# Kernel tuning notes

Measured on AMD Instinct MI355X. Metric: run time of the kernel, lower is better.

Reference implementation:

```python
import jax, jax.numpy as jnp
import numpy as np

DIM = 1024
NUM_HEADS = 16
HEAD_DIM = DIM // NUM_HEADS


def _rope(x):
    # x: (B*H, L, hd). ESM-style rotary embedding with rotate_half.
    L, hd = x.shape[1], x.shape[2]
    inv_freq = 1.0 / (10000.0 ** (jnp.arange(0, hd, 2, dtype=jnp.float32) / hd))
    t = jnp.arange(L, dtype=jnp.float32)
    freqs = t[:, None] * inv_freq[None, :]          # (L, hd/2)
    emb = jnp.concatenate([freqs, freqs], axis=-1)   # (L, hd)
    cos, sin = jnp.cos(emb), jnp.sin(emb)
    x1, x2 = jnp.split(x, 2, axis=-1)
    rot = jnp.concatenate([-x2, x1], axis=-1)
    return x * cos + rot * sin


def setup_inputs() -> dict:
    key = jax.random.key(0)
    ks = jax.random.split(key, 10)
    L, N, D = 2048, 1, DIM
    query = jax.random.normal(ks[0], (L, N, D), dtype=jnp.float32)
    asym_ids = jnp.sort(jax.random.randint(ks[1], (N, L), 0, 4), axis=-1)
    s = 0.02
    wq = s * jax.random.normal(ks[2], (D, D), dtype=jnp.float32)
    wk = s * jax.random.normal(ks[3], (D, D), dtype=jnp.float32)
    wv = s * jax.random.normal(ks[4], (D, D), dtype=jnp.float32)
    wo = s * jax.random.normal(ks[5], (D, D), dtype=jnp.float32)
    bq = s * jax.random.normal(ks[6], (D,), dtype=jnp.float32)
    bk = s * jax.random.normal(ks[7], (D,), dtype=jnp.float32)
    bv = s * jax.random.normal(ks[8], (D,), dtype=jnp.float32)
    bo = s * jax.random.normal(ks[9], (D,), dtype=jnp.float32)
    return {"query": query, "asym_ids": asym_ids, "wq": wq, "bq": bq,
            "wk": wk, "bk": bk, "wv": wv, "bv": bv, "wo": wo, "bo": bo}


def reference(query, asym_ids, wq, bq, wk, bk, wv, bv, wo, bo):
    L, N, D = query.shape
    H, hd = NUM_HEADS, HEAD_DIM
    scaling = 1.0 / np.sqrt(hd)

    q = (query @ wq.T + bq) * scaling
    k = query @ wk.T + bk
    v = query @ wv.T + bv

    def to_bh(x):  # (L, N, D) -> (N*H, L, hd)
        return x.reshape(L, N * H, hd).transpose(1, 0, 2)

    q, k, v = to_bh(q), to_bh(k), to_bh(v)

    # raw scores (pre-RoPE), rpe scores (post-RoPE)
    raw = jnp.einsum('ble,bme->blm', q, k).reshape(N, H, L, L)
    qr, kr = _rope(q), _rope(k)
    rpe = jnp.einsum('ble,bme->blm', qr, kr).reshape(N, H, L, L)

    avg = jnp.mean(rpe - raw, axis=(0, 1), keepdims=True)          # (1,1,L,L)
    asym_mask = asym_ids[:, :, None] == asym_ids[:, None, :]        # (N,L,L)
    attn_weights = jnp.where(asym_mask[:, None], rpe, raw + avg)    # (N,H,L,L)

    probs = jax.nn.softmax(attn_weights, axis=-1)
    attn = jnp.einsum('nhlm,nhme->nhle', probs, v.reshape(N, H, L, hd))
    attn = attn.transpose(2, 0, 1, 3).reshape(L, N, D)
    out = attn @ wo.T + bo
    attn_weights_avg = jnp.mean(probs, axis=1)  # (N, L, L)
    return out, attn_weights_avg
```

## Files before the change

### kernel.cpp

```cpp
#include <hip/hip_runtime.h>
#include <hip/hip_bf16.h>

#define L 2048
#define D 1024
#define NH 16
#define HD 64
#define SPLIT 4
#define JCH (L / SPLIT)
#define LOG2E 1.4426950408889634f

typedef __attribute__((ext_vector_type(8))) short bf16x8;
typedef __attribute__((ext_vector_type(4))) float f32x4;

#define MFMA(a, b, c) __builtin_amdgcn_mfma_f32_16x16x32_bf16(a, b, c, 0, 0, 0)

__device__ __forceinline__ short f2bf(float x) {
  __hip_bfloat16 h = __float2bfloat16(x);
  return *reinterpret_cast<short*>(&h);
}

__device__ __forceinline__ void gll16(const void* g, void* l) {
  __builtin_amdgcn_global_load_lds(
      (const __attribute__((address_space(1))) void*)(uintptr_t)g,
      (__attribute__((address_space(3))) void*)(unsigned)(uintptr_t)l, 16, 0, 0);
}

__global__ void prep_kernel(const float* __restrict__ q,
                            const float* __restrict__ w0, const float* __restrict__ w1,
                            const float* __restrict__ w2, const float* __restrict__ w3,
                            float* __restrict__ costab, float* __restrict__ sintab,
                            short* __restrict__ dq, short* __restrict__ d0,
                            short* __restrict__ d1, short* __restrict__ d2,
                            short* __restrict__ d3) {
  int i = blockIdx.x * 256 + threadIdx.x;
  if (i < 65536) {
    int t = i >> 5, fi = i & 31;
    float f = exp2f(-(float)fi * (13.287712379549449f / 32.0f));
    float ang = (float)t * f;
    costab[i] = cosf(ang);
    sintab[i] = sinf(ang);
    return;
  }
  int i2 = i - 65536;
  const float* src;
  short* dst;
  int off;
  if (i2 < L * D / 4) {
    src = q; dst = dq; off = i2;
  } else {
    int j = i2 - L * D / 4;
    int seg = j >> 18;
    off = j & (262144 - 1);
    src = seg == 0 ? w0 : seg == 1 ? w1 : seg == 2 ? w2 : w3;
    dst = seg == 0 ? d0 : seg == 1 ? d1 : seg == 2 ? d2 : d3;
  }
  float4 v = ((const float4*)src)[off];
  short4 o;
  o.x = f2bf(v.x); o.y = f2bf(v.y); o.z = f2bf(v.z); o.w = f2bf(v.w);
  ((short4*)dst)[off] = o;
}

__global__ __launch_bounds__(256) void proj3_kernel(
    const short* __restrict__ X,
    const short* __restrict__ Wq, const short* __restrict__ Wk, const short* __restrict__ Wv,
    const float* __restrict__ bq, const float* __restrict__ bk, const float* __restrict__ bv,
    const float* __restrict__ costab, const float* __restrict__ sintab,
    short* __restrict__ Qs, short* __restrict__ QRb, short* __restrict__ Kbb,
    short* __restrict__ KRb, short* __restrict__ Vt) {
  int mode = blockIdx.z;
  const short* W = mode == 0 ? Wq : (mode == 1 ? Wk : Wv);
  const float* bias = mode == 0 ? bq : (mode == 1 ? bk : bv);
  short* out_main = mode == 0 ? Qs : (mode == 1 ? Kbb : Vt);
  short* out_rope = mode == 0 ? QRb : KRb;

  int w = threadIdx.x >> 6, lane = threadIdx.x & 63;
  int c = lane & 15, g = lane >> 4;
  int wi0 = blockIdx.y * 128 + (w >> 1) * 64;
  int wj0 = blockIdx.x * 128 + (w & 1) * 64;

  f32x4 acc[4][4];
#pragma unroll
  for (int m = 0; m < 4; ++m)
#pragma unroll
    for (int n = 0; n < 4; ++n) acc[m][n] = (f32x4){0.f, 0.f, 0.f, 0.f};

  for (int k0 = 0; k0 < D; k0 += 32) {
    bf16x8 aF[4], bF[4];
#pragma unroll
    for (int m = 0; m < 4; ++m)
      aF[m] = *(const bf16x8*)(X + (size_t)(wi0 + m * 16 + c) * D + k0 + g * 8);
#pragma unroll
    for (int n = 0; n < 4; ++n)
      bF[n] = *(const bf16x8*)(W + (size_t)(wj0 + n * 16 + c) * D + k0 + g * 8);
#pragma unroll
    for (int m = 0; m < 4; ++m)
#pragma unroll
      for (int n = 0; n < 4; ++n) acc[m][n] = MFMA(aF[m], bF[n], acc[m][n]);
  }

  float scale = (mode == 0) ? 0.125f * LOG2E : 1.0f;
#pragma unroll
  for (int m = 0; m < 4; ++m) {
#pragma unroll
    for (int r = 0; r < 4; ++r) {
      int i = wi0 + m * 16 + g * 4 + r;
      float v4[4];
#pragma unroll
      for (int n = 0; n < 4; ++n)
        v4[n] = (acc[m][n][r] + bias[wj0 + n * 16 + c]) * scale;
      if (mode == 2) {
#pragma unroll
        for (int n = 0; n < 4; ++n) {
          int col = wj0 + n * 16 + c;
          out_main[(size_t)col * L + i] = f2bf(v4[n]);
        }
      } else {
#pragma unroll
        for (int n = 0; n < 4; ++n) {
          int col = wj0 + n * 16 + c;
          out_main[(size_t)i * D + col] = f2bf(v4[n]);
          float rot = (n < 2) ? -v4[n + 2] : v4[n - 2];
          int fidx = i * 32 + (n & 1) * 16 + c;
          float vr = v4[n] * costab[fidx] + rot * sintab[fidx];
          out_rope[(size_t)i * D + col] = f2bf(vr);
        }
      }
    }
  }
}

__global__ __launch_bounds__(256) void avg_kernel(
    const short* __restrict__ QR, const short* __restrict__ KR,
    const short* __restrict__ Qs, const short* __restrict__ Kb,
    const int* __restrict__ ids, f32x4* __restrict__ avg4) {
  int ib = blockIdx.y * 128, jb = blockIdx.x * 64;
  if (ids[ib] == ids[ib + 127] && ids[jb] == ids[jb + 63] && ids[ib] == ids[jb])
    return;

  int w = threadIdx.x >> 6, lane = threadIdx.x & 63;
  int c = lane & 15, g = lane >> 4;
  int wi0 = ib + (w >> 1) * 64;
  int wj0 = jb + (w & 1) * 32;

  f32x4 acc1[4][2], acc2[4][2];
#pragma unroll
  for (int m = 0; m < 4; ++m)
#pragma unroll
    for (int n = 0; n < 2; ++n) {
      acc1[m][n] = (f32x4){0.f, 0.f, 0.f, 0.f};
      acc2[m][n] = (f32x4){0.f, 0.f, 0.f, 0.f};
    }

  for (int k0 = 0; k0 < D; k0 += 32) {
    bf16x8 aF[4], a2F[4], bF[2], b2F[2];
#pragma unroll
    for (int m = 0; m < 4; ++m) {
      aF[m] = *(const bf16x8*)(QR + (size_t)(wi0 + m * 16 + c) * D + k0 + g * 8);
      a2F[m] = *(const bf16x8*)(Qs + (size_t)(wi0 + m * 16 + c) * D + k0 + g * 8);
    }
#pragma unroll
    for (int n = 0; n < 2; ++n) {
      bF[n] = *(const bf16x8*)(KR + (size_t)(wj0 + n * 16 + c) * D + k0 + g * 8);
      b2F[n] = *(const bf16x8*)(Kb + (size_t)(wj0 + n * 16 + c) * D + k0 + g * 8);
    }
#pragma unroll
    for (int m = 0; m < 4; ++m)
#pragma unroll
      for (int n = 0; n < 2; ++n) {
        acc1[m][n] = MFMA(aF[m], bF[n], acc1[m][n]);
        acc2[m][n] = MFMA(a2F[m], b2F[n], acc2[m][n]);
      }
  }

#pragma unroll
  for (int m = 0; m < 4; ++m)
#pragma unroll
    for (int n = 0; n < 2; ++n) {
      int j = wj0 + n * 16 + c;
      f32x4 o;
#pragma unroll
      for (int r = 0; r < 4; ++r) o[r] = (acc1[m][n][r] - acc2[m][n][r]) * 0.0625f;
      avg4[(size_t)(((wi0 + m * 16) >> 2) + g) * L + j] = o;
    }
}

__global__ __launch_bounds__(256) void flash3_kernel(
    const short* __restrict__ Qs, const short* __restrict__ Kb,
    const short* __restrict__ QR, const short* __restrict__ KR,
    const short* __restrict__ Vt, const f32x4* __restrict__ avg4,
    const int* __restrict__ ids, float* __restrict__ m_part,
    float* __restrict__ l_part, float* __restrict__ acc_part) {
  int h = blockIdx.y, sp = blockIdx.z;
  int w = threadIdx.x >> 6, lane = threadIdx.x & 63;
  int c = lane & 15, g = lane >> 4;
  int i0 = blockIdx.x * 64 + w * 16;
  int hk = h * 64;

  __shared__ short kb_lds[2][64 * 64];
  __shared__ short kr_lds[2][64 * 64];
  __shared__ short plds[4][16][64];

  int srow = lane >> 3;
  int sxor = (lane & 7) ^ srow;
  int r0a = w * 16, r0b = w * 16 + 8;

  bf16x8 qA[2], qrA[2];
  {
    const short* qp = Qs + (size_t)(i0 + c) * D + hk + g * 8;
    const short* qrp = QR + (size_t)(i0 + c) * D + hk + g * 8;
    qA[0] = *(const bf16x8*)qp;   qA[1] = *(const bf16x8*)(qp + 32);
    qrA[0] = *(const bf16x8*)qrp; qrA[1] = *(const bf16x8*)(qrp + 32);
  }

  int idi[4];
  float mrun[4], lsum[4];
  f32x4 acc[4];
#pragma unroll
  for (int r = 0; r < 4; ++r) {
    idi[r] = ids[i0 + g * 4 + r];
    mrun[r] = -3.0e38f;
    lsum[r] = 0.f;
  }
#pragma unroll
  for (int n = 0; n < 4; ++n) acc[n] = (f32x4){0.f, 0.f, 0.f, 0.f};

  int ifirst = __shfl(idi[0], 0);
  bool iu = __all((idi[0] == idi[1]) & (idi[1] == idi[2]) & (idi[2] == idi[3]) &
                  (idi[0] == ifirst));

  const f32x4* avrow = avg4 + (size_t)((i0 >> 2) + g) * L;
  int jbase = sp * JCH;
  const int NT = JCH / 64;

  gll16(Kb + (size_t)(jbase + r0a + srow) * D + hk + sxor * 8, &kb_lds[0][r0a * 64]);
  gll16(Kb + (size_t)(jbase + r0b + srow) * D + hk + sxor * 8, &kb_lds[0][r0b * 64]);
  gll16(KR + (size_t)(jbase + r0a + srow) * D + hk + sxor * 8, &kr_lds[0][r0a * 64]);
  gll16(KR + (size_t)(jbase + r0b + srow) * D + hk + sxor * 8, &kr_lds[0][r0b * 64]);

  f32x4 avn[4];
  int idjn[4];
#pragma unroll
  for (int sub = 0; sub < 4; ++sub) {
    avn[sub] = avrow[jbase + sub * 16 + c];
    idjn[sub] = ids[jbase + sub * 16 + c];
  }
  __syncthreads();

  int cur = 0;
  for (int jt = 0; jt < NT; ++jt) {
    int jb = jbase + jt * 64;

    if (jt + 1 < NT) {
      int jn = jb + 64;
      short* kd = &kb_lds[cur ^ 1][0];
      short* rd = &kr_lds[cur ^ 1][0];
      gll16(Kb + (size_t)(jn + r0a + srow) * D + hk + sxor * 8, kd + r0a * 64);
      gll16(Kb + (size_t)(jn + r0b + srow) * D + hk + sxor * 8, kd + r0b * 64);
      gll16(KR + (size_t)(jn + r0a + srow) * D + hk + sxor * 8, rd + r0a * 64);
      gll16(KR + (size_t)(jn + r0b + srow) * D + hk + sxor * 8, rd + r0b * 64);
    }

    bf16x8 vf0[4], vf1[4];
#pragma unroll
    for (int n = 0; n < 4; ++n) {
      const short* vp = Vt + (size_t)(hk + n * 16 + c) * L + jb + g * 8;
      vf0[n] = *(const bf16x8*)vp;
      vf1[n] = *(const bf16x8*)(vp + 32);
    }

    f32x4 av[4];
    int idj[4];
#pragma unroll
    for (int sub = 0; sub < 4; ++sub) { av[sub] = avn[sub]; idj[sub] = idjn[sub]; }
    if (jt + 1 < NT) {
#pragma unroll
      for (int sub = 0; sub < 4; ++sub) {
        avn[sub] = avrow[jb + 64 + sub * 16 + c];
        idjn[sub] = ids[jb + 64 + sub * 16 + c];
      }
    }

    int jfirst = __shfl(idj[0], 0);
    bool ju = __all((idj[0] == idj[1]) & (idj[1] == idj[2]) & (idj[2] == idj[3]) &
                    (idj[0] == jfirst));

    const short* kbb = &kb_lds[cur][c * 64];
    const short* krb = &kr_lds[cur][c * 64];
    int co0 = (g ^ (c & 7)) * 8;
    int co1 = ((4 + g) ^ (c & 7)) * 8;

    float t[4][4];
    if (iu && ju && ifirst == jfirst) {
#pragma unroll
      for (int sub = 0; sub < 4; ++sub) {
        bf16x8 kr0 = *(const bf16x8*)(krb + sub * 1024 + co0);
        bf16x8 kr1 = *(const bf16x8*)(krb + sub * 1024 + co1);
        f32x4 z = (f32x4){0.f, 0.f, 0.f, 0.f};
        f32x4 rp = MFMA(qrA[1], kr1, MFMA(qrA[0], kr0, z));
#pragma unroll
        for (int r = 0; r < 4; ++r) t[sub][r] = rp[r];
      }
    } else if (iu && ju) {
#pragma unroll
      for (int sub = 0; sub < 4; ++sub) {
        bf16x8 k0 = *(const bf16x8*)(kbb + sub * 1024 + co0);
        bf16x8 k1 = *(const bf16x8*)(kbb + sub * 1024 + co1);
        f32x4 z = (f32x4){0.f, 0.f, 0.f, 0.f};
        f32x4 rw = MFMA(qA[1], k1, MFMA(qA[0], k0, z));
#pragma unroll
        for (int r = 0; r < 4; ++r) t[sub][r] = rw[r] + av[sub][r];
      }
    } else {
#pragma unroll
      for (int sub = 0; sub < 4; ++sub) {
        bf16x8 k0 = *(const bf16x8*)(kbb + sub * 1024 + co0);
        bf16x8 k1 = *(const bf16x8*)(kbb + sub * 1024 + co1);
        bf16x8 kr0 = *(const bf16x8*)(krb + sub * 1024 + co0);
        bf16x8 kr1 = *(const bf16x8*)(krb + sub * 1024 + co1);
        f32x4 z = (f32x4){0.f, 0.f, 0.f, 0.f};
        f32x4 rw = MFMA(qA[1], k1, MFMA(qA[0], k0, z));
        f32x4 rp = MFMA(qrA[1], kr1, MFMA(qrA[0], kr0, z));
#pragma unroll
        for (int r = 0; r < 4; ++r)
          t[sub][r] = (idi[r] == idj[sub]) ? rp[r] : (rw[r] + av[sub][r]);
      }
    }

    float tm[4];
#pragma unroll
    for (int r = 0; r < 4; ++r)
      tm[r] = fmaxf(fmaxf(t[0][r], t[1][r]), fmaxf(t[2][r], t[3][r]));
    bool ok = (tm[0] <= mrun[0] + 8.f) && (tm[1] <= mrun[1] + 8.f) &&
              (tm[2] <= mrun[2] + 8.f) && (tm[3] <= mrun[3] + 8.f);
    if (!__all(ok)) {
#pragma unroll
      for (int r = 0; r < 4; ++r) {
        float m2 = tm[r];
#pragma unroll
        for (int d = 1; d < 16; d <<= 1) m2 = fmaxf(m2, __shfl_xor(m2, d));
        float mn = fmaxf(mrun[r], m2);
        float so = exp2f(mrun[r] - mn);
        mrun[r] = mn;
        lsum[r] *= so;
#pragma unroll
        for (int n = 0; n < 4; ++n) acc[n][r] *= so;
      }
    }

#pragma unroll
    for (int sub = 0; sub < 4; ++sub)
#pragma unroll
      for (int r = 0; r < 4; ++r) {
        float p = exp2f(t[sub][r] - mrun[r]);
        lsum[r] += p;
        int prow = g * 4 + r;
        plds[w][prow][(sub * 16 + c) ^ ((prow & 7) << 3)] = f2bf(p);
      }

    {
      int pc0 = (g * 8) ^ ((c & 7) << 3);
      int pc1 = (32 + g * 8) ^ ((c & 7) << 3);
      bf16x8 pa = *(const bf16x8*)(&plds[w][c][pc0]);
#pragma unroll
      for (int n = 0; n < 4; ++n) acc[n] = MFMA(pa, vf0[n], acc[n]);
      bf16x8 pb = *(const bf16x8*)(&plds[w][c][pc1]);
#pragma unroll
      for (int n = 0; n < 4; ++n) acc[n] = MFMA(pb, vf1[n], acc[n]);
    }

    __syncthreads();
    cur ^= 1;
  }

#pragma unroll
  for (int r = 0; r < 4; ++r) {
#pragma unroll
    for (int d = 1; d < 16; d <<= 1) lsum[r] += __shfl_xor(lsum[r], d);
  }
  size_t sb = (size_t)(sp * NH + h) * L;
  if (c == 0) {
#pragma unroll
    for (int r = 0; r < 4; ++r) {
      m_part[sb + i0 + g * 4 + r] = mrun[r];
      l_part[sb + i0 + g * 4 + r] = lsum[r];
    }
  }
#pragma unroll
  for (int n = 0; n < 4; ++n)
#pragma unroll
    for (int r = 0; r < 4; ++r)
      acc_part[(sb + i0 + g * 4 + r) * HD + n * 16 + c] = acc[n][r];
}

__global__ void merge_kernel(const float* __restrict__ m_part,
                             const float* __restrict__ l_part,
                             const float* __restrict__ acc_part,
                             float* __restrict__ mfin, float* __restrict__ lfin,
                             short* __restrict__ attn_bf) {
  int idx = blockIdx.x * 256 + threadIdx.x;
  int d = idx & (HD - 1);
  int hi = idx >> 6;
  int i = hi & (L - 1), h = hi >> 11;
  float m4 = -3.0e38f;
#pragma unroll
  for (int s = 0; s < SPLIT; ++s)
    m4 = fmaxf(m4, m_part[(size_t)(s * NH + h) * L + i]);
  float l = 0.f, o = 0.f;
#pragma unroll
  for (int s = 0; s < SPLIT; ++s) {
    size_t sb = (size_t)(s * NH + h) * L + i;
    float e = exp2f(m_part[sb] - m4);
    l += l_part[sb] * e;
    o += acc_part[sb * HD + d] * e;
  }
  attn_bf[(size_t)i * D + h * HD + d] = f2bf(o / l);
  if (d == 0) { mfin[h * L + i] = m4; lfin[h * L + i] = l; }
}

__global__ __launch_bounds__(256) void pavg_kernel(
    const short* __restrict__ Qs, const short* __restrict__ Kb,
    const short* __restrict__ QR, const short* __restrict__ KR,
    const f32x4* __restrict__ avg4, const int* __restrict__ ids,
    const float* __restrict__ m_ws, const float* __restrict__ l_ws,
    float* __restrict__ out1) {
  int j0 = blockIdx.x * 64;
  int iblk = blockIdx.y * 64;
  int w = threadIdx.x >> 6, lane = threadIdx.x & 63;
  int c = lane & 15, g = lane >> 4;
  int i0 = iblk + w * 16;

  __shared__ short kb_lds[2][64 * 64];
  __shared__ short kr_lds[2][64 * 64];
  __shared__ float mS[NH][64], lS[NH][64];

  int srow = lane >> 3;
  int sxor = (lane & 7) ^ srow;
  int r0a = w * 16, r0b = w * 16 + 8;

  int si0 = ids[iblk], si1 = ids[iblk + 63];
  int sj0 = ids[j0], sj1 = ids[j0 + 63];
  int mode = (si0 == si1 && sj0 == sj1) ? ((si0 == sj0) ? 0 : 1) : 2;

  for (int idx = threadIdx.x; idx < NH * 64; idx += 256) {
    int hh = idx >> 6, rr = idx & 63;
    mS[hh][rr] = m_ws[hh * L + iblk + rr];
    lS[hh][rr] = 1.0f / l_ws[hh * L + iblk + rr];
  }

  if (mode != 0) {
    gll16(Kb + (size_t)(j0 + r0a + srow) * D + sxor * 8, &kb_lds[0][r0a * 64]);
    gll16(Kb + (size_t)(j0 + r0b + srow) * D + sxor * 8, &kb_lds[0][r0b * 64]);
  }
  if (mode != 1) {
    gll16(KR + (size_t)(j0 + r0a + srow) * D + sxor * 8, &kr_lds[0][r0a * 64]);
    gll16(KR + (size_t)(j0 + r0b + srow) * D + sxor * 8, &kr_lds[0][r0b * 64]);
  }

  int idi[4], idj[4];
  f32x4 av[4];
  {
    const f32x4* avrow = avg4 + (size_t)((i0 >> 2) + g) * L;
#pragma unroll
    for (int sub = 0; sub < 4; ++sub) {
      av[sub] = avrow[j0 + sub * 16 + c];
      idj[sub] = ids[j0 + sub * 16 + c];
    }
#pragma unroll
    for (int r = 0; r < 4; ++r) idi[r] = ids[i0 + g * 4 + r];
  }

  f32x4 psum[4];
#pragma unroll
  for (int sub = 0; sub < 4; ++sub) psum[sub] = (f32x4){0.f, 0.f, 0.f, 0.f};

  const short* qbase = Qs + (size_t)(i0 + c) * D + g * 8;
  const short* qrbase = QR + (size_t)(i0 + c) * D + g * 8;

  bf16x8 nq0, nq1, nqr0, nqr1;
  if (mode != 0) { nq0 = *(const bf16x8*)qbase; nq1 = *(const bf16x8*)(qbase + 32); }
  if (mode != 1) { nqr0 = *(const bf16x8*)qrbase; nqr1 = *(const bf16x8*)(qrbase + 32); }

  __syncthreads();

  int cur = 0;
#pragma unroll 1
  for (int hh = 0; hh < NH; ++hh) {
    if (hh + 1 < NH) {
      int hkn = (hh + 1) * 64;
      short* kd = &kb_lds[cur ^ 1][0];
      short* rd = &kr_lds[cur ^ 1][0];
      if (mode != 0) {
        gll16(Kb + (size_t)(j0 + r0a + srow) * D + hkn + sxor * 8, kd + r0a * 64);
        gll16(Kb + (size_t)(j0 + r0b + srow) * D + hkn + sxor * 8, kd + r0b * 64);
      }
      if (mode != 1) {
        gll16(KR + (size_t)(j0 + r0a + srow) * D + hkn + sxor * 8, rd + r0a * 64);
        gll16(KR + (size_t)(j0 + r0b + srow) * D + hkn + sxor * 8, rd + r0b * 64);
      }
    }

    bf16x8 q0 = nq0, q1 = nq1, qr0 = nqr0, qr1 = nqr1;
    if (hh + 1 < NH) {
      int hkn = (hh + 1) * 64;
      if (mode != 0) {
        nq0 = *(const bf16x8*)(qbase + hkn);
        nq1 = *(const bf16x8*)(qbase + hkn + 32);
      }
      if (mode != 1) {
        nqr0 = *(const bf16x8*)(qrbase + hkn);
        nqr1 = *(const bf16x8*)(qrbase + hkn + 32);
      }
    }

    const short* kbb = &kb_lds[cur][c * 64];
    const short* krb = &kr_lds[cur][c * 64];
    int co0 = (g ^ (c & 7)) * 8;
    int co1 = ((4 + g) ^ (c & 7)) * 8;

    f32x4 m4 = *(const f32x4*)(&mS[hh][w * 16 + g * 4]);
    f32x4 l4 = *(const f32x4*)(&lS[hh][w * 16 + g * 4]);

    if (mode == 0) {
#pragma unroll
      for (int sub = 0; sub < 4; ++sub) {
        bf16x8 kr0 = *(const bf16x8*)(krb + sub * 1024 + co0);
        bf16x8 kr1 = *(const bf16x8*)(krb + sub * 1024 + co1);
        f32x4 z = (f32x4){0.f, 0.f, 0.f, 0.f};
        f32x4 rp = MFMA(qr1, kr1, MFMA(qr0, kr0, z));
#pragma unroll
        for (int r = 0; r < 4; ++r)
          psum[sub][r] += exp2f(rp[r] - m4[r]) * l4[r];
      }
    } else if (mode == 1) {
#pragma unroll
      for (int sub = 0; sub < 4; ++sub) {
        bf16x8 k0 = *(const bf16x8*)(kbb + sub * 1024 + co0);
        bf16x8 k1 = *(const bf16x8*)(kbb + sub * 1024 + co1);
        f32x4 z = (f32x4){0.f, 0.f, 0.f, 0.f};
        f32x4 rw = MFMA(q1, k1, MFMA(q0, k0, z));
#pragma unroll
        for (int r = 0; r < 4; ++r)
          psum[sub][r] += exp2f(rw[r] + av[sub][r] - m4[r]) * l4[r];
      }
    } else {
#pragma unroll
      for (int sub = 0; sub < 4; ++sub) {
        bf16x8 k0 = *(const bf16x8*)(kbb + sub * 1024 + co0);
        bf16x8 k1 = *(const bf16x8*)(kbb + sub * 1024 + co1);
        bf16x8 kr0 = *(const bf16x8*)(krb + sub * 1024 + co0);
        bf16x8 kr1 = *(const bf16x8*)(krb + sub * 1024 + co1);
        f32x4 z = (f32x4){0.f, 0.f, 0.f, 0.f};
        f32x4 rw = MFMA(q1, k1, MFMA(q0, k0, z));
        f32x4 rp = MFMA(qr1, kr1, MFMA(qr0, kr0, z));
#pragma unroll
        for (int r = 0; r < 4; ++r) {
          float s = (idi[r] == idj[sub]) ? rp[r] : (rw[r] + av[sub][r]);
          psum[sub][r] += exp2f(s - m4[r]) * l4[r];
        }
      }
    }

    __syncthreads();
    cur ^= 1;
  }

#pragma unroll
  for (int sub = 0; sub < 4; ++sub)
#pragma unroll
    for (int r = 0; r < 4; ++r)
      out1[(size_t)(i0 + g * 4 + r) * L + j0 + sub * 16 + c] = psum[sub][r] * 0.0625f;
}

__global__ __launch_bounds__(256) void outproj_kernel(
    const short* __restrict__ A, const short* __restrict__ W,
    const float* __restrict__ bias, float* __restrict__ out) {
  int w = threadIdx.x >> 6, lane = threadIdx.x & 63;
  int c = lane & 15, g = lane >> 4;
  int wi0 = blockIdx.y * 64 + (w >> 1) * 32;
  int wj0 = blockIdx.x * 64 + (w & 1) * 32;

  f32x4 acc[2][2];
#pragma unroll
  for (int m = 0; m < 2; ++m)
#pragma unroll
    for (int n = 0; n < 2; ++n) acc[m][n] = (f32x4){0.f, 0.f, 0.f, 0.f};

  for (int k0 = 0; k0 < D; k0 += 32) {
    bf16x8 aF[2], bF[2];
#pragma unroll
    for (int m = 0; m < 2; ++m)
      aF[m] = *(const bf16x8*)(A + (size_t)(wi0 + m * 16 + c) * D + k0 + g * 8);
#pragma unroll
    for (int n = 0; n < 2; ++n)
      bF[n] = *(const bf16x8*)(W + (size_t)(wj0 + n * 16 + c) * D + k0 + g * 8);
#pragma unroll
    for (int m = 0; m < 2; ++m)
#pragma unroll
      for (int n = 0; n < 2; ++n) acc[m][n] = MFMA(aF[m], bF[n], acc[m][n]);
  }

#pragma unroll
  for (int m = 0; m < 2; ++m)
#pragma unroll
    for (int n = 0; n < 2; ++n)
#pragma unroll
      for (int r = 0; r < 4; ++r) {
        int i = wi0 + m * 16 + g * 4 + r;
        int col = wj0 + n * 16 + c;
        out[(size_t)i * D + col] = acc[m][n][r] + bias[col];
      }
}

extern "C" void kernel_launch(void* const* d_in, const int* in_sizes, int n_in,
                              void* d_out, int out_size, void* d_ws, size_t ws_size,
                              hipStream_t stream) {
  const float* query = (const float*)d_in[0];
  const int* ids = (const int*)d_in[1];
  const float* wq = (const float*)d_in[2];
  const float* bq = (const float*)d_in[3];
  const float* wk = (const float*)d_in[4];
  const float* bk = (const float*)d_in[5];
  const float* wv = (const float*)d_in[6];
  const float* bv = (const float*)d_in[7];
  const float* wo = (const float*)d_in[8];
  const float* bo = (const float*)d_in[9];

  char* p = (char*)d_ws;
  auto carve = [&](size_t bytes) {
    char* r = p;
    p += (bytes + 255) & ~(size_t)255;
    return r;
  };
  short* Xbf = (short*)carve((size_t)L * D * 2);
  short* Wqb = (short*)carve((size_t)D * D * 2);
  short* Wkb = (short*)carve((size_t)D * D * 2);
  short* Wvb = (short*)carve((size_t)D * D * 2);
  short* Wob = (short*)carve((size_t)D * D * 2);
  short* Qs = (short*)carve((size_t)L * D * 2);
  short* QRb = (short*)carve((size_t)L * D * 2);
  short* Kbb = (short*)carve((size_t)L * D * 2);
  short* KRb = (short*)carve((size_t)L * D * 2);
  short* Vt = (short*)carve((size_t)L * D * 2);
  f32x4* avg4 = (f32x4*)carve((size_t)L * L * 4);
  float* m_ws = (float*)carve((size_t)NH * L * 4);
  float* l_ws = (float*)carve((size_t)NH * L * 4);
  short* attn_bf = (short*)carve((size_t)L * D * 2);
  float* costab = (float*)carve((size_t)L * 32 * 4);
  float* sintab = (float*)carve((size_t)L * 32 * 4);
  float* m_part = (float*)carve((size_t)SPLIT * NH * L * 4);
  float* l_part = (float*)carve((size_t)SPLIT * NH * L * 4);
  float* acc_part = (float*)carve((size_t)SPLIT * NH * L * HD * 4);

  float* out0 = (float*)d_out;
  float* out1 = out0 + (size_t)L * D;

  prep_kernel<<<(65536 + L * D / 4 + 4 * (D * D / 4)) / 256, 256, 0, stream>>>(
      query, wq, wk, wv, wo, costab, sintab, Xbf, Wqb, Wkb, Wvb, Wob);

  proj3_kernel<<<dim3(D / 128, L / 128, 3), 256, 0, stream>>>(
      Xbf, Wqb, Wkb, Wvb, bq, bk, bv, costab, sintab, Qs, QRb, Kbb, KRb, Vt);

  avg_kernel<<<dim3(L / 64, L / 128), 256, 0, stream>>>(QRb, KRb, Qs, Kbb, ids, avg4);

  flash3_kernel<<<dim3(L / 64, NH, SPLIT), 256, 0, stream>>>(
      Qs, Kbb, QRb, KRb, Vt, avg4, ids, m_part, l_part, acc_part);

  merge_kernel<<<(NH * L * HD) / 256, 256, 0, stream>>>(m_part, l_part, acc_part,
                                                        m_ws, l_ws, attn_bf);

  pavg_kernel<<<dim3(L / 64, L / 64), 256, 0, stream>>>(Qs, Kbb, QRb, KRb, avg4, ids,
                                                        m_ws, l_ws, out1);

  outproj_kernel<<<dim3(D / 64, L / 64), 256, 0, stream>>>(attn_bf, Wob, bo, out0);
}
```

Baseline: 347.6 us.

## Classify tiles by block-level asym ids and skip unneeded K/KR and avg loads

The tile mode (same-chain rope only, cross-chain raw+avg, or mixed) is now decided per 64-row block and 64-column tile from the first and last sorted ids, replacing per-wave shuffle/all votes. Only the K or rotated-K tile that the mode needs is prefetched into LDS, and the avg prefetch is skipped for same-chain tiles. SPLIT is also halved, so each block walks twice as many j-tiles with fewer partial results to merge. The classification depends on the asym ids being sorted, which setup_inputs does guarantee, and fewer column splits reduce parallelism.

```diff
diff --git a/kernel.cpp b/kernel.cpp
--- a/kernel.cpp
+++ b/kernel.cpp
@@ -5,7 +5,7 @@
 #define D 1024
 #define NH 16
 #define HD 64
-#define SPLIT 4
+#define SPLIT 2
 #define JCH (L / SPLIT)
 #define LOG2E 1.4426950408889634f
 
@@ -224,40 +224,56 @@
 #pragma unroll
   for (int n = 0; n < 4; ++n) acc[n] = (f32x4){0.f, 0.f, 0.f, 0.f};
 
-  int ifirst = __shfl(idi[0], 0);
-  bool iu = __all((idi[0] == idi[1]) & (idi[1] == idi[2]) & (idi[2] == idi[3]) &
-                  (idi[0] == ifirst));
+  int ib0 = blockIdx.x * 64;
+  int bva = ids[ib0];
+  bool biu = (bva == ids[ib0 + 63]);
 
   const f32x4* avrow = avg4 + (size_t)((i0 >> 2) + g) * L;
   int jbase = sp * JCH;
   const int NT = JCH / 64;
 
-  gll16(Kb + (size_t)(jbase + r0a + srow) * D + hk + sxor * 8, &kb_lds[0][r0a * 64]);
-  gll16(Kb + (size_t)(jbase + r0b + srow) * D + hk + sxor * 8, &kb_lds[0][r0b * 64]);
-  gll16(KR + (size_t)(jbase + r0a + srow) * D + hk + sxor * 8, &kr_lds[0][r0a * 64]);
-  gll16(KR + (size_t)(jbase + r0b + srow) * D + hk + sxor * 8, &kr_lds[0][r0b * 64]);
+  int modeN;
+  {
+    int mj0 = ids[jbase], mj1 = ids[jbase + 63];
+    modeN = (!biu || mj0 != mj1) ? 2 : (mj0 == bva ? 0 : 1);
+  }
+  if (modeN != 0) {
+    gll16(Kb + (size_t)(jbase + r0a + srow) * D + hk + sxor * 8, &kb_lds[0][r0a * 64]);
+    gll16(Kb + (size_t)(jbase + r0b + srow) * D + hk + sxor * 8, &kb_lds[0][r0b * 64]);
+  }
+  if (modeN != 1) {
+    gll16(KR + (size_t)(jbase + r0a + srow) * D + hk + sxor * 8, &kr_lds[0][r0a * 64]);
+    gll16(KR + (size_t)(jbase + r0b + srow) * D + hk + sxor * 8, &kr_lds[0][r0b * 64]);
+  }
 
   f32x4 avn[4];
   int idjn[4];
 #pragma unroll
   for (int sub = 0; sub < 4; ++sub) {
-    avn[sub] = avrow[jbase + sub * 16 + c];
     idjn[sub] = ids[jbase + sub * 16 + c];
+    if (modeN != 0) avn[sub] = avrow[jbase + sub * 16 + c];
   }
   __syncthreads();
 
   int cur = 0;
   for (int jt = 0; jt < NT; ++jt) {
     int jb = jbase + jt * 64;
+    int modeC = modeN;
 
     if (jt + 1 < NT) {
       int jn = jb + 64;
+      int mj0 = ids[jn], mj1 = ids[jn + 63];
+      modeN = (!biu || mj0 != mj1) ? 2 : (mj0 == bva ? 0 : 1);
       short* kd = &kb_lds[cur ^ 1][0];
       short* rd = &kr_lds[cur ^ 1][0];
-      gll16(Kb + (size_t)(jn + r0a + srow) * D + hk + sxor * 8, kd + r0a * 64);
-      gll16(Kb + (size_t)(jn + r0b + srow) * D + hk + sxor * 8, kd + r0b * 64);
-      gll16(KR + (size_t)(jn + r0a + srow) * D + hk + sxor * 8, rd + r0a * 64);
-      gll16(KR + (size_t)(jn + r0b + srow) * D + hk + sxor * 8, rd + r0b * 64);
+      if (modeN != 0) {
+        gll16(Kb + (size_t)(jn + r0a + srow) * D + hk + sxor * 8, kd + r0a * 64);
+        gll16(Kb + (size_t)(jn + r0b + srow) * D + hk + sxor * 8, kd + r0b * 64);
+      }
+      if (modeN != 1) {
+        gll16(KR + (size_t)(jn + r0a + srow) * D + hk + sxor * 8, rd + r0a * 64);
+        gll16(KR + (size_t)(jn + r0b + srow) * D + hk + sxor * 8, rd + r0b * 64);
+      }
     }
 
     bf16x8 vf0[4], vf1[4];
@@ -275,14 +291,10 @@
     if (jt + 1 < NT) {
 #pragma unroll
       for (int sub = 0; sub < 4; ++sub) {
-        avn[sub] = avrow[jb + 64 + sub * 16 + c];
         idjn[sub] = ids[jb + 64 + sub * 16 + c];
-      }
-    }
-
-    int jfirst = __shfl(idj[0], 0);
-    bool ju = __all((idj[0] == idj[1]) & (idj[1] == idj[2]) & (idj[2] == idj[3]) &
-                    (idj[0] == jfirst));
+        if (modeN != 0) avn[sub] = avrow[jb + 64 + sub * 16 + c];
+      }
+    }
 
     const short* kbb = &kb_lds[cur][c * 64];
     const short* krb = &kr_lds[cur][c * 64];
@@ -290,7 +302,7 @@
     int co1 = ((4 + g) ^ (c & 7)) * 8;
 
     float t[4][4];
-    if (iu && ju && ifirst == jfirst) {
+    if (modeC == 0) {
 #pragma unroll
       for (int sub = 0; sub < 4; ++sub) {
         bf16x8 kr0 = *(const bf16x8*)(krb + sub * 1024 + co0);
@@ -300,7 +312,7 @@
 #pragma unroll
         for (int r = 0; r < 4; ++r) t[sub][r] = rp[r];
       }
-    } else if (iu && ju) {
+    } else if (modeC == 1) {
 #pragma unroll
       for (int sub = 0; sub < 4; ++sub) {
         bf16x8 k0 = *(const bf16x8*)(kbb + sub * 1024 + co0);
```

Result: slower. 380.2 us (+9.4%).

## Shrink projection/avg tiles and merge out-projection into pavg launch

Applied to the files above, without the earlier changes.

Halves the per-block tile of the QKV projection and the avg-difference GEMM so each launches more blocks and fills more compute units. The pavg and output-projection kernels are combined into one launch of 1536 blocks: the first 1024 do the probability-average work and the rest do the out-projection GEMM. This removes one launch and lets the two independent tails run side by side. Smaller tiles mean less register reuse and more global loads per MFMA. The fused kernel carries the LDS allocation of the pavg path even for GEMM blocks, which may lower occupancy.

```diff
diff --git a/kernel.cpp b/kernel.cpp
--- a/kernel.cpp
+++ b/kernel.cpp
@@ -75,32 +75,32 @@
 
   int w = threadIdx.x >> 6, lane = threadIdx.x & 63;
   int c = lane & 15, g = lane >> 4;
-  int wi0 = blockIdx.y * 128 + (w >> 1) * 64;
-  int wj0 = blockIdx.x * 128 + (w & 1) * 64;
-
-  f32x4 acc[4][4];
-#pragma unroll
-  for (int m = 0; m < 4; ++m)
+  int wi0 = blockIdx.y * 128 + w * 32;
+  int wj0 = blockIdx.x * 64;
+
+  f32x4 acc[2][4];
+#pragma unroll
+  for (int m = 0; m < 2; ++m)
 #pragma unroll
     for (int n = 0; n < 4; ++n) acc[m][n] = (f32x4){0.f, 0.f, 0.f, 0.f};
 
   for (int k0 = 0; k0 < D; k0 += 32) {
-    bf16x8 aF[4], bF[4];
-#pragma unroll
-    for (int m = 0; m < 4; ++m)
+    bf16x8 aF[2], bF[4];
+#pragma unroll
+    for (int m = 0; m < 2; ++m)
       aF[m] = *(const bf16x8*)(X + (size_t)(wi0 + m * 16 + c) * D + k0 + g * 8);
 #pragma unroll
     for (int n = 0; n < 4; ++n)
       bF[n] = *(const bf16x8*)(W + (size_t)(wj0 + n * 16 + c) * D + k0 + g * 8);
 #pragma unroll
-    for (int m = 0; m < 4; ++m)
+    for (int m = 0; m < 2; ++m)
 #pragma unroll
       for (int n = 0; n < 4; ++n) acc[m][n] = MFMA(aF[m], bF[n], acc[m][n]);
   }
 
   float scale = (mode == 0) ? 0.125f * LOG2E : 1.0f;
 #pragma unroll
-  for (int m = 0; m < 4; ++m) {
+  for (int m = 0; m < 2; ++m) {
 #pragma unroll
     for (int r = 0; r < 4; ++r) {
       int i = wi0 + m * 16 + g * 4 + r;
@@ -133,55 +133,45 @@
     const short* __restrict__ QR, const short* __restrict__ KR,
     const short* __restrict__ Qs, const short* __restrict__ Kb,
     const int* __restrict__ ids, f32x4* __restrict__ avg4) {
-  int ib = blockIdx.y * 128, jb = blockIdx.x * 64;
-  if (ids[ib] == ids[ib + 127] && ids[jb] == ids[jb + 63] && ids[ib] == ids[jb])
+  int ib = blockIdx.y * 64, jb = blockIdx.x * 64;
+  if (ids[ib] == ids[ib + 63] && ids[jb] == ids[jb + 63] && ids[ib] == ids[jb])
     return;
 
   int w = threadIdx.x >> 6, lane = threadIdx.x & 63;
   int c = lane & 15, g = lane >> 4;
-  int wi0 = ib + (w >> 1) * 64;
-  int wj0 = jb + (w & 1) * 32;
-
-  f32x4 acc1[4][2], acc2[4][2];
-#pragma unroll
-  for (int m = 0; m < 4; ++m)
-#pragma unroll
-    for (int n = 0; n < 2; ++n) {
-      acc1[m][n] = (f32x4){0.f, 0.f, 0.f, 0.f};
-      acc2[m][n] = (f32x4){0.f, 0.f, 0.f, 0.f};
-    }
+  int wi0 = ib + w * 16;
+
+  f32x4 acc1[4], acc2[4];
+#pragma unroll
+  for (int n = 0; n < 4; ++n) {
+    acc1[n] = (f32x4){0.f, 0.f, 0.f, 0.f};
+    acc2[n] = (f32x4){0.f, 0.f, 0.f, 0.f};
+  }
 
   for (int k0 = 0; k0 < D; k0 += 32) {
-    bf16x8 aF[4], a2F[4], bF[2], b2F[2];
-#pragma unroll
-    for (int m = 0; m < 4; ++m) {
-      aF[m] = *(const bf16x8*)(QR + (size_t)(wi0 + m * 16 + c) * D + k0 + g * 8);
-      a2F[m] = *(const bf16x8*)(Qs + (size_t)(wi0 + m * 16 + c) * D + k0 + g * 8);
-    }
-#pragma unroll
-    for (int n = 0; n < 2; ++n) {
-      bF[n] = *(const bf16x8*)(KR + (size_t)(wj0 + n * 16 + c) * D + k0 + g * 8);
-      b2F[n] = *(const bf16x8*)(Kb + (size_t)(wj0 + n * 16 + c) * D + k0 + g * 8);
-    }
-#pragma unroll
-    for (int m = 0; m < 4; ++m)
-#pragma unroll
-      for (int n = 0; n < 2; ++n) {
-        acc1[m][n] = MFMA(aF[m], bF[n], acc1[m][n]);
-        acc2[m][n] = MFMA(a2F[m], b2F[n], acc2[m][n]);
-      }
-  }
-
-#pragma unroll
-  for (int m = 0; m < 4; ++m)
-#pragma unroll
-    for (int n = 0; n < 2; ++n) {
-      int j = wj0 + n * 16 + c;
-      f32x4 o;
-#pragma unroll
-      for (int r = 0; r < 4; ++r) o[r] = (acc1[m][n][r] - acc2[m][n][r]) * 0.0625f;
-      avg4[(size_t)(((wi0 + m * 16) >> 2) + g) * L + j] = o;
-    }
+    bf16x8 aF = *(const bf16x8*)(QR + (size_t)(wi0 + c) * D + k0 + g * 8);
+    bf16x8 a2F = *(const bf16x8*)(Qs + (size_t)(wi0 + c) * D + k0 + g * 8);
+    bf16x8 bF[4], b2F[4];
+#pragma unroll
+    for (int n = 0; n < 4; ++n) {
+      bF[n] = *(const bf16x8*)(KR + (size_t)(jb + n * 16 + c) * D + k0 + g * 8);
+      b2F[n] = *(const bf16x8*)(Kb + (size_t)(jb + n * 16 + c) * D + k0 + g * 8);
+    }
+#pragma unroll
+    for (int n = 0; n < 4; ++n) {
+      acc1[n] = MFMA(aF, bF[n], acc1[n]);
+      acc2[n] = MFMA(a2F, b2F[n], acc2[n]);
+    }
+  }
+
+#pragma unroll
+  for (int n = 0; n < 4; ++n) {
+    int j = jb + n * 16 + c;
+    f32x4 o;
+#pragma unroll
+    for (int r = 0; r < 4; ++r) o[r] = (acc1[n][r] - acc2[n][r]) * 0.0625f;
+    avg4[(size_t)((wi0 >> 2) + g) * L + j] = o;
+  }
 }
 
 __global__ __launch_bounds__(256) void flash3_kernel(
@@ -417,21 +407,63 @@
   if (d == 0) { mfin[h * L + i] = m4; lfin[h * L + i] = l; }
 }
 
-__global__ __launch_bounds__(256) void pavg_kernel(
+__global__ __launch_bounds__(256) void pavgout_kernel(
     const short* __restrict__ Qs, const short* __restrict__ Kb,
     const short* __restrict__ QR, const short* __restrict__ KR,
     const f32x4* __restrict__ avg4, const int* __restrict__ ids,
     const float* __restrict__ m_ws, const float* __restrict__ l_ws,
-    float* __restrict__ out1) {
-  int j0 = blockIdx.x * 64;
-  int iblk = blockIdx.y * 64;
-  int w = threadIdx.x >> 6, lane = threadIdx.x & 63;
-  int c = lane & 15, g = lane >> 4;
-  int i0 = iblk + w * 16;
-
+    float* __restrict__ out1,
+    const short* __restrict__ A, const short* __restrict__ W,
+    const float* __restrict__ bias, float* __restrict__ out0) {
   __shared__ short kb_lds[2][64 * 64];
   __shared__ short kr_lds[2][64 * 64];
   __shared__ float mS[NH][64], lS[NH][64];
+
+  int bid = blockIdx.x;
+  int w = threadIdx.x >> 6, lane = threadIdx.x & 63;
+  int c = lane & 15, g = lane >> 4;
+
+  if (bid >= 1024) {
+    int idx = bid - 1024;
+    int wj0 = (idx & 15) * 64 + (w & 1) * 32;
+    int wi0 = (idx >> 4) * 64 + (w >> 1) * 32;
+
+    f32x4 acc[2][2];
+#pragma unroll
+    for (int m = 0; m < 2; ++m)
+#pragma unroll
+      for (int n = 0; n < 2; ++n) acc[m][n] = (f32x4){0.f, 0.f, 0.f, 0.f};
+
+    for (int k0 = 0; k0 < D; k0 += 32) {
+      bf16x8 aF[2], bF[2];
+#pragma unroll
+      for (int m = 0; m < 2; ++m)
+        aF[m] = *(const bf16x8*)(A + (size_t)(wi0 + m * 16 + c) * D + k0 + g * 8);
+#pragma unroll
+      for (int n = 0; n < 2; ++n)
+        bF[n] = *(const bf16x8*)(W + (size_t)(wj0 + n * 16 + c) * D + k0 + g * 8);
+#pragma unroll
+      for (int m = 0; m < 2; ++m)
+#pragma unroll
+        for (int n = 0; n < 2; ++n) acc[m][n] = MFMA(aF[m], bF[n], acc[m][n]);
+    }
+
+#pragma unroll
+    for (int m = 0; m < 2; ++m)
+#pragma unroll
+      for (int n = 0; n < 2; ++n)
+#pragma unroll
+        for (int r = 0; r < 4; ++r) {
+          int i = wi0 + m * 16 + g * 4 + r;
+          int col = wj0 + n * 16 + c;
+          out0[(size_t)i * D + col] = acc[m][n][r] + bias[col];
+        }
+    return;
+  }
+
+  int j0 = (bid & 31) * 64;
+  int iblk = (bid >> 5) * 64;
+  int i0 = iblk + w * 16;
 
   int srow = lane >> 3;
   int sxor = (lane & 7) ^ srow;
@@ -569,46 +601,6 @@
 #pragma unroll
     for (int r = 0; r < 4; ++r)
       out1[(size_t)(i0 + g * 4 + r) * L + j0 + sub * 16 + c] = psum[sub][r] * 0.0625f;
-}
-
-__global__ __launch_bounds__(256) void outproj_kernel(
-    const short* __restrict__ A, const short* __restrict__ W,
-    const float* __restrict__ bias, float* __restrict__ out) {
-  int w = threadIdx.x >> 6, lane = threadIdx.x & 63;
-  int c = lane & 15, g = lane >> 4;
-  int wi0 = blockIdx.y * 64 + (w >> 1) * 32;
-  int wj0 = blockIdx.x * 64 + (w & 1) * 32;
-
-  f32x4 acc[2][2];
-#pragma unroll
-  for (int m = 0; m < 2; ++m)
-#pragma unroll
-    for (int n = 0; n < 2; ++n) acc[m][n] = (f32x4){0.f, 0.f, 0.f, 0.f};
-
-  for (int k0 = 0; k0 < D; k0 += 32) {
-    bf16x8 aF[2], bF[2];
-#pragma unroll
-    for (int m = 0; m < 2; ++m)
-      aF[m] = *(const bf16x8*)(A + (size_t)(wi0 + m * 16 + c) * D + k0 + g * 8);
-#pragma unroll
-    for (int n = 0; n < 2; ++n)
-      bF[n] = *(const bf16x8*)(W + (size_t)(wj0 + n * 16 + c) * D + k0 + g * 8);
-#pragma unroll
-    for (int m = 0; m < 2; ++m)
-#pragma unroll
-      for (int n = 0; n < 2; ++n) acc[m][n] = MFMA(aF[m], bF[n], acc[m][n]);
-  }
-
-#pragma unroll
-  for (int m = 0; m < 2; ++m)
-#pragma unroll
-    for (int n = 0; n < 2; ++n)
-#pragma unroll
-      for (int r = 0; r < 4; ++r) {
-        int i = wi0 + m * 16 + g * 4 + r;
-        int col = wj0 + n * 16 + c;
-        out[(size_t)i * D + col] = acc[m][n][r] + bias[col];
-      }
 }
 
 extern "C" void kernel_launch(void* const* d_in, const int* in_sizes, int n_in,
@@ -657,10 +649,10 @@
   prep_kernel<<<(65536 + L * D / 4 + 4 * (D * D / 4)) / 256, 256, 0, stream>>>(
       query, wq, wk, wv, wo, costab, sintab, Xbf, Wqb, Wkb, Wvb, Wob);
 
-  proj3_kernel<<<dim3(D / 128, L / 128, 3), 256, 0, stream>>>(
+  proj3_kernel<<<dim3(D / 64, L / 128, 3), 256, 0, stream>>>(
       Xbf, Wqb, Wkb, Wvb, bq, bk, bv, costab, sintab, Qs, QRb, Kbb, KRb, Vt);
 
-  avg_kernel<<<dim3(L / 64, L / 128), 256, 0, stream>>>(QRb, KRb, Qs, Kbb, ids, avg4);
+  avg_kernel<<<dim3(L / 64, L / 64), 256, 0, stream>>>(QRb, KRb, Qs, Kbb, ids, avg4);
 
   flash3_kernel<<<dim3(L / 64, NH, SPLIT), 256, 0, stream>>>(
       Qs, Kbb, QRb, KRb, Vt, avg4, ids, m_part, l_part, acc_part);
@@ -668,8 +660,6 @@
   merge_kernel<<<(NH * L * HD) / 256, 256, 0, stream>>>(m_part, l_part, acc_part,
                                                         m_ws, l_ws, attn_bf);
 
-  pavg_kernel<<<dim3(L / 64, L / 64), 256, 0, stream>>>(Qs, Kbb, QRb, KRb, avg4, ids,
-                                                        m_ws, l_ws, out1);
-
-  outproj_kernel<<<dim3(D / 64, L / 64), 256, 0, stream>>>(attn_bf, Wob, bo, out0);
-}
+  pavgout_kernel<<<1536, 256, 0, stream>>>(Qs, Kbb, QRb, KRb, avg4, ids,
+                                           m_ws, l_ws, out1, attn_bf, Wob, bo, out0);
+}
```

After: 397.8 us. 1.14x slower.

## Merge output projection into pavg launch and shrink proj3 per-wave tile

Applied to the files above, without the earlier changes.

The pavg kernel and the output-projection GEMM become one launch. Block IDs below 1024 do the probability-average work and the remaining 512 blocks compute the output projection, so both independent jobs can share the GPU and one launch plus its tail disappears. Separately, proj3 now gives each wave a 32x64 tile instead of 64x64 and doubles the grid, which raises block count and occupancy at the cost of less operand reuse per wave. The fused kernel carries pavg's shared-memory allocation into the GEMM blocks, which may limit their occupancy.

```diff
diff --git a/kernel.cpp b/kernel.cpp
--- a/kernel.cpp
+++ b/kernel.cpp
@@ -75,32 +75,32 @@
 
   int w = threadIdx.x >> 6, lane = threadIdx.x & 63;
   int c = lane & 15, g = lane >> 4;
-  int wi0 = blockIdx.y * 128 + (w >> 1) * 64;
-  int wj0 = blockIdx.x * 128 + (w & 1) * 64;
-
-  f32x4 acc[4][4];
-#pragma unroll
-  for (int m = 0; m < 4; ++m)
+  int wi0 = blockIdx.y * 128 + w * 32;
+  int wj0 = blockIdx.x * 64;
+
+  f32x4 acc[2][4];
+#pragma unroll
+  for (int m = 0; m < 2; ++m)
 #pragma unroll
     for (int n = 0; n < 4; ++n) acc[m][n] = (f32x4){0.f, 0.f, 0.f, 0.f};
 
   for (int k0 = 0; k0 < D; k0 += 32) {
-    bf16x8 aF[4], bF[4];
-#pragma unroll
-    for (int m = 0; m < 4; ++m)
+    bf16x8 aF[2], bF[4];
+#pragma unroll
+    for (int m = 0; m < 2; ++m)
       aF[m] = *(const bf16x8*)(X + (size_t)(wi0 + m * 16 + c) * D + k0 + g * 8);
 #pragma unroll
     for (int n = 0; n < 4; ++n)
       bF[n] = *(const bf16x8*)(W + (size_t)(wj0 + n * 16 + c) * D + k0 + g * 8);
 #pragma unroll
-    for (int m = 0; m < 4; ++m)
+    for (int m = 0; m < 2; ++m)
 #pragma unroll
       for (int n = 0; n < 4; ++n) acc[m][n] = MFMA(aF[m], bF[n], acc[m][n]);
   }
 
   float scale = (mode == 0) ? 0.125f * LOG2E : 1.0f;
 #pragma unroll
-  for (int m = 0; m < 4; ++m) {
+  for (int m = 0; m < 2; ++m) {
 #pragma unroll
     for (int r = 0; r < 4; ++r) {
       int i = wi0 + m * 16 + g * 4 + r;
@@ -417,21 +417,63 @@
   if (d == 0) { mfin[h * L + i] = m4; lfin[h * L + i] = l; }
 }
 
-__global__ __launch_bounds__(256) void pavg_kernel(
+__global__ __launch_bounds__(256) void pavgout_kernel(
     const short* __restrict__ Qs, const short* __restrict__ Kb,
     const short* __restrict__ QR, const short* __restrict__ KR,
     const f32x4* __restrict__ avg4, const int* __restrict__ ids,
     const float* __restrict__ m_ws, const float* __restrict__ l_ws,
-    float* __restrict__ out1) {
-  int j0 = blockIdx.x * 64;
-  int iblk = blockIdx.y * 64;
-  int w = threadIdx.x >> 6, lane = threadIdx.x & 63;
-  int c = lane & 15, g = lane >> 4;
-  int i0 = iblk + w * 16;
-
+    float* __restrict__ out1,
+    const short* __restrict__ A, const short* __restrict__ W,
+    const float* __restrict__ bias, float* __restrict__ out0) {
   __shared__ short kb_lds[2][64 * 64];
   __shared__ short kr_lds[2][64 * 64];
   __shared__ float mS[NH][64], lS[NH][64];
+
+  int bid = blockIdx.x;
+  int w = threadIdx.x >> 6, lane = threadIdx.x & 63;
+  int c = lane & 15, g = lane >> 4;
+
+  if (bid >= 1024) {
+    int idx = bid - 1024;
+    int wj0 = (idx & 15) * 64 + (w & 1) * 32;
+    int wi0 = (idx >> 4) * 64 + (w >> 1) * 32;
+
+    f32x4 acc[2][2];
+#pragma unroll
+    for (int m = 0; m < 2; ++m)
+#pragma unroll
+      for (int n = 0; n < 2; ++n) acc[m][n] = (f32x4){0.f, 0.f, 0.f, 0.f};
+
+    for (int k0 = 0; k0 < D; k0 += 32) {
+      bf16x8 aF[2], bF[2];
+#pragma unroll
+      for (int m = 0; m < 2; ++m)
+        aF[m] = *(const bf16x8*)(A + (size_t)(wi0 + m * 16 + c) * D + k0 + g * 8);
+#pragma unroll
+      for (int n = 0; n < 2; ++n)
+        bF[n] = *(const bf16x8*)(W + (size_t)(wj0 + n * 16 + c) * D + k0 + g * 8);
+#pragma unroll
+      for (int m = 0; m < 2; ++m)
+#pragma unroll
+        for (int n = 0; n < 2; ++n) acc[m][n] = MFMA(aF[m], bF[n], acc[m][n]);
+    }
+
+#pragma unroll
+    for (int m = 0; m < 2; ++m)
+#pragma unroll
+      for (int n = 0; n < 2; ++n)
+#pragma unroll
+        for (int r = 0; r < 4; ++r) {
+          int i = wi0 + m * 16 + g * 4 + r;
+          int col = wj0 + n * 16 + c;
+          out0[(size_t)i * D + col] = acc[m][n][r] + bias[col];
+        }
+    return;
+  }
+
+  int j0 = (bid & 31) * 64;
+  int iblk = (bid >> 5) * 64;
+  int i0 = iblk + w * 16;
 
   int srow = lane >> 3;
   int sxor = (lane & 7) ^ srow;
@@ -569,46 +611,6 @@
 #pragma unroll
     for (int r = 0; r < 4; ++r)
       out1[(size_t)(i0 + g * 4 + r) * L + j0 + sub * 16 + c] = psum[sub][r] * 0.0625f;
-}
-
-__global__ __launch_bounds__(256) void outproj_kernel(
-    const short* __restrict__ A, const short* __restrict__ W,
-    const float* __restrict__ bias, float* __restrict__ out) {
-  int w = threadIdx.x >> 6, lane = threadIdx.x & 63;
-  int c = lane & 15, g = lane >> 4;
-  int wi0 = blockIdx.y * 64 + (w >> 1) * 32;
-  int wj0 = blockIdx.x * 64 + (w & 1) * 32;
-
-  f32x4 acc[2][2];
-#pragma unroll
-  for (int m = 0; m < 2; ++m)
-#pragma unroll
-    for (int n = 0; n < 2; ++n) acc[m][n] = (f32x4){0.f, 0.f, 0.f, 0.f};
-
-  for (int k0 = 0; k0 < D; k0 += 32) {
-    bf16x8 aF[2], bF[2];
-#pragma unroll
-    for (int m = 0; m < 2; ++m)
-      aF[m] = *(const bf16x8*)(A + (size_t)(wi0 + m * 16 + c) * D + k0 + g * 8);
-#pragma unroll
-    for (int n = 0; n < 2; ++n)
-      bF[n] = *(const bf16x8*)(W + (size_t)(wj0 + n * 16 + c) * D + k0 + g * 8);
-#pragma unroll
-    for (int m = 0; m < 2; ++m)
-#pragma unroll
-      for (int n = 0; n < 2; ++n) acc[m][n] = MFMA(aF[m], bF[n], acc[m][n]);
-  }
-
-#pragma unroll
-  for (int m = 0; m < 2; ++m)
-#pragma unroll
-    for (int n = 0; n < 2; ++n)
-#pragma unroll
-      for (int r = 0; r < 4; ++r) {
-        int i = wi0 + m * 16 + g * 4 + r;
-        int col = wj0 + n * 16 + c;
-        out[(size_t)i * D + col] = acc[m][n][r] + bias[col];
-      }
 }
 
 extern "C" void kernel_launch(void* const* d_in, const int* in_sizes, int n_in,
@@ -657,7 +659,7 @@
   prep_kernel<<<(65536 + L * D / 4 + 4 * (D * D / 4)) / 256, 256, 0, stream>>>(
       query, wq, wk, wv, wo, costab, sintab, Xbf, Wqb, Wkb, Wvb, Wob);
 
-  proj3_kernel<<<dim3(D / 128, L / 128, 3), 256, 0, stream>>>(
+  proj3_kernel<<<dim3(D / 64, L / 128, 3), 256, 0, stream>>>(
       Xbf, Wqb, Wkb, Wvb, bq, bk, bv, costab, sintab, Qs, QRb, Kbb, KRb, Vt);
 
   avg_kernel<<<dim3(L / 64, L / 128), 256, 0, stream>>>(QRb, KRb, Qs, Kbb, ids, avg4);
@@ -668,8 +670,6 @@
   merge_kernel<<<(NH * L * HD) / 256, 256, 0, stream>>>(m_part, l_part, acc_part,
                                                         m_ws, l_ws, attn_bf);
 
-  pavg_kernel<<<dim3(L / 64, L / 64), 256, 0, stream>>>(Qs, Kbb, QRb, KRb, avg4, ids,
-                                                        m_ws, l_ws, out1);
-
-  outproj_kernel<<<dim3(D / 64, L / 64), 256, 0, stream>>>(attn_bf, Wob, bo, out0);
-}
+  pavgout_kernel<<<1536, 256, 0, stream>>>(Qs, Kbb, QRb, KRb, avg4, ids,
+                                           m_ws, l_ws, out1, attn_bf, Wob, bo, out0);
+}
```

New measurement: 343.5 us, median of 3. No clear change (-1.2%).
